# Optimization experiments

Measured on AMD Instinct MI355X. Metric: run time of the kernel, lower is better.

## Reference

```python
import jax, jax.numpy as jnp
import numpy as np

B = 131072      # flattened batch of item embeddings
E = 256         # e_dim; x has 2*E features (src half, rec half)
NQ = 4          # residual quantizer levels per branch
NE = 256        # codebook size per level
BETA = 0.25


def setup_inputs() -> dict:
    key = jax.random.key(0)
    k1, k2, k3 = jax.random.split(key, 3)
    x = jax.random.normal(k1, (B, 2 * E), dtype=jnp.float32)
    src_codebooks = jax.random.normal(k2, (NQ, NE, E), dtype=jnp.float32)
    rec_codebooks = jax.random.normal(k3, (NQ, NE, E), dtype=jnp.float32)
    return {"x": x, "src_codebooks": src_codebooks, "rec_codebooks": rec_codebooks}


def _vq(residual, cb):
    # residual: [B, E], cb: [NE, E]
    # squared euclidean distances via expanded form (GEMM-dominated)
    d = (jnp.sum(residual * residual, axis=1, keepdims=True)
         - 2.0 * (residual @ cb.T)
         + jnp.sum(cb * cb, axis=1)[None, :])          # [B, NE]
    idx = jnp.argmin(d, axis=1)                          # [B]
    x_q = cb[idx]                                        # gather [B, E]
    loss = (jnp.mean((jax.lax.stop_gradient(x_q) - residual) ** 2)
            + BETA * jnp.mean((x_q - jax.lax.stop_gradient(residual)) ** 2))
    # straight-through estimator
    x_q = residual + jax.lax.stop_gradient(x_q - residual)
    return x_q, loss, idx


def _rq(x_part, codebooks):
    # sequential residual VQ chain over NQ levels (small fixed unroll)
    residual = x_part
    x_q = jnp.zeros_like(x_part)
    losses, indices = [], []
    for i in range(codebooks.shape[0]):
        x_res, l, idx = _vq(residual, codebooks[i])
        residual = residual - x_res
        x_q = x_q + x_res
        losses.append(l)
        indices.append(idx)
    return x_q, jnp.stack(losses), jnp.stack(indices, axis=-1)


def reference(x, src_codebooks, rec_codebooks):
    src_x_q, src_l, src_idx = _rq(x[:, :E], src_codebooks)
    rec_x_q, rec_l, rec_idx = _rq(x[:, E:], rec_codebooks)
    mean_loss = jnp.mean(jnp.concatenate([src_l, rec_l]))
    return ((src_x_q, rec_x_q), mean_loss, (src_idx, rec_idx))
```

## Files before the change

### kernel.cpp

```cpp
#include <hip/hip_runtime.h>
#include <hip/hip_bf16.h>
#include <hip/hip_fp16.h>
#include <cstdint>
#include <cstddef>

#define NB   131072
#define ED   256
#define NQL  4
#define NEC  256

typedef _Float16 f16;
typedef f16  f16x8 __attribute__((ext_vector_type(8)));
typedef float f32x4 __attribute__((ext_vector_type(4)));

static constexpr float FMAXV = 3.402823466e+38f;
static constexpr float TAU   = 0.15625f;

static constexpr size_t OFF_REC  = (size_t)NB * ED;
static constexpr size_t OFF_LOSS = 2 * (size_t)NB * ED;
static constexpr size_t OFF_SIDX = OFF_LOSS + 1;
static constexpr size_t OFF_RIDX = OFF_SIDX + (size_t)NB * NQL;

static constexpr size_t WS_LOSS = 0;
static constexpr size_t WS_NORM = 256;
static constexpr size_t WS_CBH  = 256 + 8 * 256 * 4;

__global__ void kPrep(const float* __restrict__ cbS, const float* __restrict__ cbR,
                      float* __restrict__ norms, double* __restrict__ lossAcc) {
  const int cbi = blockIdx.x;
  const int j   = threadIdx.x;
  if (cbi == 0 && j < 8) lossAcc[j] = 0.0;
  const float* row = (cbi < 4 ? cbS : cbR) + ((size_t)(cbi & 3) * NEC + j) * ED;
  float acc = 0.f;
  for (int k = 0; k < ED; k += 4) {
    float4 v = *(const float4*)(row + k);
    acc += v.x * v.x + v.y * v.y + v.z * v.z + v.w * v.w;
  }
  norms[cbi * NEC + j] = acc - 256.0f;
}

__global__ void kConvH(const float* __restrict__ cbS, const float* __restrict__ cbR,
                       f16* __restrict__ cbH) {
  const int f   = blockIdx.x * 256 + threadIdx.x;
  const int cbi = f >> 16;
  const int rem = f & 65535;
  const float v = (cbi < 4 ? cbS + ((size_t)cbi << 16) : cbR + ((size_t)(cbi - 4) << 16))[rem];
  cbH[f] = (f16)v;
}

__device__ __forceinline__ float pk(float v, int j) {
  return __uint_as_float((__float_as_uint(v) & ~255u) | (unsigned)j);
}
__device__ __forceinline__ float unpv(float k) {
  return __uint_as_float(__float_as_uint(k) & ~255u);
}
__device__ __forceinline__ void ins3(float& s0, float& s1, float& s2, float k) {
  float t0 = fmaxf(s0, k); s0 = fminf(s0, k);
  float t1 = fmaxf(s1, t0); s1 = fminf(s1, t0);
  s2 = fminf(s2, t1);
}
__device__ __forceinline__ void mrg3(float& a0, float& a1, float& a2,
                                     float b0, float b1, float b2) {
  float x  = fmaxf(a0, b0);
  float c0 = fminf(a0, b0);
  float m1 = fminf(a1, b1), M1 = fmaxf(a1, b1);
  float c1 = fminf(fminf(x, a1), b1);
  float c2 = fminf(fminf(fmaxf(x, m1), M1), fminf(a2, b2));
  a0 = c0; a1 = c1; a2 = c2;
}

__global__ __launch_bounds__(256, 2)
void kMain(const float* __restrict__ x,
           const float* __restrict__ cbS,
           const float* __restrict__ cbR,
           const f16*  __restrict__ cbH,
           const float* __restrict__ norms,
           double* __restrict__ lossAcc,
           float* __restrict__ out) {
  __shared__ __align__(16) char  RhBuf[64 * 512];
  __shared__ __align__(16) float keybuf[64][4][4];
  __shared__ float redS[4];

  const int tid   = threadIdx.x;
  const int lane  = tid & 63;
  const int w     = tid >> 6;
  const int it_o  = tid >> 2;
  const int kq    = tid & 3;
  const int b0    = blockIdx.x * 64;
  const int l15   = lane & 15;
  const int l4    = lane >> 4;

  float res[64];
  float lossReg = 0.f;

#pragma unroll 1
  for (int br = 0; br < 2; ++br) {
    const float* cbf32 = br ? cbR : cbS;

    {
      const float* xp = x + (size_t)(b0 + it_o) * (2 * ED) + br * ED + kq * 64;
#pragma unroll
      for (int i = 0; i < 16; ++i) {
        float4 v = *(const float4*)(xp + 4 * i);
        res[4 * i + 0] = v.x; res[4 * i + 1] = v.y;
        res[4 * i + 2] = v.z; res[4 * i + 3] = v.w;
      }
    }

#pragma unroll 1
    for (int lev = 0; lev < NQL; ++lev) {
      const int cbi = br * 4 + lev;
      const float* nrm = norms + (size_t)cbi * NEC;

#pragma unroll
      for (int c = 0; c < 8; ++c) {
        f16x8 h;
#pragma unroll
        for (int u = 0; u < 8; ++u) h[u] = (f16)res[c * 8 + u];
        int off = it_o * 512 + kq * 128 + c * 16;
        off ^= (it_o & 7) << 4;
        *(f16x8*)&RhBuf[off] = h;
      }
      __syncthreads();

      const f16* cbh = cbH + ((size_t)cbi << 16);

      f32x4 acc[4][4];
#pragma unroll
      for (int mt = 0; mt < 4; ++mt)
#pragma unroll
        for (int nt = 0; nt < 4; ++nt) { f32x4 z = {0.f, 0.f, 0.f, 0.f}; acc[mt][nt] = z; }

#pragma unroll 2
      for (int ks = 0; ks < 8; ++ks) {
        f16x8 A[4], Bf[4];
#pragma unroll
        for (int mt = 0; mt < 4; ++mt) {
          const int it = mt * 16 + l15;
          const int offA = (it * 512 + ks * 64 + l4 * 16) ^ ((it & 7) << 4);
          A[mt] = *(const f16x8*)&RhBuf[offA];
        }
#pragma unroll
        for (int nt = 0; nt < 4; ++nt) {
          const int j = (w * 4 + nt) * 16 + l15;
          Bf[nt] = *(const f16x8*)&cbh[(size_t)j * ED + ks * 32 + l4 * 8];
        }
#pragma unroll
        for (int mt = 0; mt < 4; ++mt)
#pragma unroll
          for (int nt = 0; nt < 4; ++nt)
            acc[mt][nt] = __builtin_amdgcn_mfma_f32_16x16x32_f16(Bf[nt], A[mt], acc[mt][nt], 0, 0, 0);
      }

      float4 nvq[4];
#pragma unroll
      for (int nt = 0; nt < 4; ++nt)
        nvq[nt] = *(const float4*)&nrm[(w * 4 + nt) * 16 + l4 * 4];

#pragma unroll
      for (int mt = 0; mt < 4; ++mt) {
        float s0 = FMAXV, s1 = FMAXV, s2 = FMAXV;
#pragma unroll
        for (int nt = 0; nt < 4; ++nt) {
#pragma unroll
          for (int r = 0; r < 4; ++r) {
            const int j = (w * 4 + nt) * 16 + l4 * 4 + r;
            const float nr = (r == 0 ? nvq[nt].x : r == 1 ? nvq[nt].y
                              : r == 2 ? nvq[nt].z : nvq[nt].w);
            ins3(s0, s1, s2, pk(fmaf(-2.f, acc[mt][nt][r], nr), j));
          }
        }
        {
          float b0k = __shfl_xor(s0, 16), b1k = __shfl_xor(s1, 16), b2k = __shfl_xor(s2, 16);
          mrg3(s0, s1, s2, b0k, b1k, b2k);
          b0k = __shfl_xor(s0, 32); b1k = __shfl_xor(s1, 32); b2k = __shfl_xor(s2, 32);
          mrg3(s0, s1, s2, b0k, b1k, b2k);
        }
        if (l4 == 0) {
          float4 v; v.x = s0; v.y = s1; v.z = s2; v.w = FMAXV;
          *(float4*)&keybuf[mt * 16 + l15][w][0] = v;
        }
      }
      __syncthreads();

      int jm;
      {
        float4 v = *(const float4*)&keybuf[it_o][kq][0];
        float s0 = v.x, s1 = v.y, s2 = v.z;
        {
          float b0k = __shfl_xor(s0, 1), b1k = __shfl_xor(s1, 1), b2k = __shfl_xor(s2, 1);
          mrg3(s0, s1, s2, b0k, b1k, b2k);
          b0k = __shfl_xor(s0, 2); b1k = __shfl_xor(s1, 2); b2k = __shfl_xor(s2, 2);
          mrg3(s0, s1, s2, b0k, b1k, b2k);
        }
        jm = (int)(__float_as_uint(s0) & 255u);
        const float gap = unpv(s1) - unpv(s0);
        if (gap < TAU) {
          const int cand[3] = { jm,
                                (int)(__float_as_uint(s1) & 255u),
                                (int)(__float_as_uint(s2) & 255u) };
          float bestd = FMAXV; int bestj = 0;
#pragma unroll 1
          for (int cc = 0; cc < 3; ++cc) {
            const int j = cand[cc];
            const float* row = cbf32 + ((size_t)lev * NEC + j) * ED + kq * 64;
            float p = 0.f;
#pragma unroll
            for (int i = 0; i < 16; ++i) {
              float4 q = *(const float4*)(row + 4 * i);
              p = fmaf(res[4 * i + 0], q.x, p);
              p = fmaf(res[4 * i + 1], q.y, p);
              p = fmaf(res[4 * i + 2], q.z, p);
              p = fmaf(res[4 * i + 3], q.w, p);
            }
            p += __shfl_xor(p, 1);
            p += __shfl_xor(p, 2);
            const float d = fmaf(-2.f, p, nrm[j]);
            if (d < bestd || (d == bestd && j < bestj)) { bestd = d; bestj = j; }
          }
          jm = bestj;
        }
        if (kq == 0) {
          const size_t ioff = (br ? OFF_RIDX : OFF_SIDX) + (size_t)(b0 + it_o) * NQL + lev;
          out[ioff] = (float)jm;
        }
      }

      {
        const float* crow = cbf32 + ((size_t)lev * NEC + jm) * ED + kq * 64;
#pragma unroll
        for (int i = 0; i < 16; ++i) {
          float4 q = *(const float4*)(crow + 4 * i);
#pragma unroll
          for (int u = 0; u < 4; ++u) {
            float cv = (u == 0 ? q.x : u == 1 ? q.y : u == 2 ? q.z : q.w);
            float r  = res[4 * i + u];
            float dd = cv - r;
            lossReg = fmaf(dd, dd, lossReg);
            float xr = r + dd;
            res[4 * i + u] = r - xr;
          }
        }
      }
    }

    {
      const float* xp = x + (size_t)(b0 + it_o) * (2 * ED) + br * ED + kq * 64;
      float* op = out + (br ? OFF_REC : 0) + (size_t)(b0 + it_o) * ED + kq * 64;
#pragma unroll
      for (int i = 0; i < 16; ++i) {
        float4 xv = *(const float4*)(xp + 4 * i);
        float4 o;
        o.x = xv.x - res[4 * i + 0];
        o.y = xv.y - res[4 * i + 1];
        o.z = xv.z - res[4 * i + 2];
        o.w = xv.w - res[4 * i + 3];
        *(float4*)(op + 4 * i) = o;
      }
    }
  }

#pragma unroll
  for (int d = 1; d < 64; d <<= 1) lossReg += __shfl_xor(lossReg, d);
  if (lane == 0) redS[w] = lossReg;
  __syncthreads();
  if (tid == 0)
    atomicAdd(&lossAcc[0], (double)((redS[0] + redS[1]) + (redS[2] + redS[3])));
}

__global__ void kFin(const double* __restrict__ lossAcc, float* __restrict__ out) {
  if (blockIdx.x == 0 && threadIdx.x == 0) {
    out[OFF_LOSS] = (float)(lossAcc[0] * 1.25 / ((double)NB * ED) / 8.0);
  }
}

extern "C" void kernel_launch(void* const* d_in, const int* in_sizes, int n_in,
                              void* d_out, int out_size, void* d_ws, size_t ws_size,
                              hipStream_t stream) {
  const float* x   = (const float*)d_in[0];
  const float* cbS = (const float*)d_in[1];
  const float* cbR = (const float*)d_in[2];
  float* out = (float*)d_out;
  char*  ws  = (char*)d_ws;

  double* lossAcc = (double*)(ws + WS_LOSS);
  float*  norms   = (float*)(ws + WS_NORM);
  f16*    cbH     = (f16*)(ws + WS_CBH);

  hipLaunchKernelGGL(kPrep,  dim3(8),    dim3(256), 0, stream, cbS, cbR, norms, lossAcc);
  hipLaunchKernelGGL(kConvH, dim3(2048), dim3(256), 0, stream, cbS, cbR, cbH);
  hipLaunchKernelGGL(kMain,  dim3(NB / 64), dim3(256), 0, stream,
                     x, cbS, cbR, cbH, norms, lossAcc, out);
  hipLaunchKernelGGL(kFin,   dim3(1),    dim3(64),  0, stream, lossAcc, out);
}
```

Before: 580.8 us.

## Halve rows per block to cut registers and raise occupancy to three blocks

Each block now handles 32 rows instead of 64, with 8 threads per row owning 32 features each. This halves the per-thread residual register array and the MFMA accumulator tile, and shrinks LDS buffers. Launch bounds now request 3 blocks per CU, and the grid doubles, with the aim of more waves in flight to hide latency. In exchange, each codebook fragment loaded from global/L2 is reused over half as many rows, which doubles codebook traffic per row. The k-loop unroll drops to 1 and an extra barrier is added between branches.

```diff
diff --git a/kernel.cpp b/kernel.cpp
--- a/kernel.cpp
+++ b/kernel.cpp
@@ -69,7 +69,7 @@
   a0 = c0; a1 = c1; a2 = c2;
 }
 
-__global__ __launch_bounds__(256, 2)
+__global__ __launch_bounds__(256, 3)
 void kMain(const float* __restrict__ x,
            const float* __restrict__ cbS,
            const float* __restrict__ cbR,
@@ -77,20 +77,20 @@
            const float* __restrict__ norms,
            double* __restrict__ lossAcc,
            float* __restrict__ out) {
-  __shared__ __align__(16) char  RhBuf[64 * 512];
-  __shared__ __align__(16) float keybuf[64][4][4];
+  __shared__ __align__(16) char  RhBuf[32 * 512];
+  __shared__ __align__(16) float keybuf[32][4][4];
   __shared__ float redS[4];
 
   const int tid   = threadIdx.x;
   const int lane  = tid & 63;
   const int w     = tid >> 6;
-  const int it_o  = tid >> 2;
-  const int kq    = tid & 3;
-  const int b0    = blockIdx.x * 64;
+  const int it_o  = tid >> 3;
+  const int kg    = tid & 7;
+  const int b0    = blockIdx.x * 32;
   const int l15   = lane & 15;
   const int l4    = lane >> 4;
 
-  float res[64];
+  float res[32];
   float lossReg = 0.f;
 
 #pragma unroll 1
@@ -98,9 +98,9 @@
     const float* cbf32 = br ? cbR : cbS;
 
     {
-      const float* xp = x + (size_t)(b0 + it_o) * (2 * ED) + br * ED + kq * 64;
-#pragma unroll
-      for (int i = 0; i < 16; ++i) {
+      const float* xp = x + (size_t)(b0 + it_o) * (2 * ED) + br * ED + kg * 32;
+#pragma unroll
+      for (int i = 0; i < 8; ++i) {
         float4 v = *(const float4*)(xp + 4 * i);
         res[4 * i + 0] = v.x; res[4 * i + 1] = v.y;
         res[4 * i + 2] = v.z; res[4 * i + 3] = v.w;
@@ -111,62 +111,56 @@
     for (int lev = 0; lev < NQL; ++lev) {
       const int cbi = br * 4 + lev;
       const float* nrm = norms + (size_t)cbi * NEC;
-
-#pragma unroll
-      for (int c = 0; c < 8; ++c) {
+      const f16*   cbh = cbH + ((size_t)cbi << 16);
+
+#pragma unroll
+      for (int c = 0; c < 4; ++c) {
         f16x8 h;
 #pragma unroll
         for (int u = 0; u < 8; ++u) h[u] = (f16)res[c * 8 + u];
-        int off = it_o * 512 + kq * 128 + c * 16;
+        int off = it_o * 512 + kg * 64 + c * 16;
         off ^= (it_o & 7) << 4;
         *(f16x8*)&RhBuf[off] = h;
       }
       __syncthreads();
 
-      const f16* cbh = cbH + ((size_t)cbi << 16);
-
-      f32x4 acc[4][4];
-#pragma unroll
-      for (int mt = 0; mt < 4; ++mt)
+      f32x4 acc[2][4];
+#pragma unroll
+      for (int mt = 0; mt < 2; ++mt)
 #pragma unroll
         for (int nt = 0; nt < 4; ++nt) { f32x4 z = {0.f, 0.f, 0.f, 0.f}; acc[mt][nt] = z; }
 
-#pragma unroll 2
+#pragma unroll 1
       for (int ks = 0; ks < 8; ++ks) {
-        f16x8 A[4], Bf[4];
-#pragma unroll
-        for (int mt = 0; mt < 4; ++mt) {
+        f16x8 A[2], Bf[4];
+#pragma unroll
+        for (int mt = 0; mt < 2; ++mt) {
           const int it = mt * 16 + l15;
           const int offA = (it * 512 + ks * 64 + l4 * 16) ^ ((it & 7) << 4);
           A[mt] = *(const f16x8*)&RhBuf[offA];
         }
 #pragma unroll
         for (int nt = 0; nt < 4; ++nt) {
-          const int j = (w * 4 + nt) * 16 + l15;
+          const int j = w * 64 + nt * 16 + l15;
           Bf[nt] = *(const f16x8*)&cbh[(size_t)j * ED + ks * 32 + l4 * 8];
         }
 #pragma unroll
-        for (int mt = 0; mt < 4; ++mt)
+        for (int mt = 0; mt < 2; ++mt)
 #pragma unroll
           for (int nt = 0; nt < 4; ++nt)
             acc[mt][nt] = __builtin_amdgcn_mfma_f32_16x16x32_f16(Bf[nt], A[mt], acc[mt][nt], 0, 0, 0);
       }
 
-      float4 nvq[4];
-#pragma unroll
-      for (int nt = 0; nt < 4; ++nt)
-        nvq[nt] = *(const float4*)&nrm[(w * 4 + nt) * 16 + l4 * 4];
-
-#pragma unroll
-      for (int mt = 0; mt < 4; ++mt) {
+#pragma unroll
+      for (int mt = 0; mt < 2; ++mt) {
         float s0 = FMAXV, s1 = FMAXV, s2 = FMAXV;
 #pragma unroll
         for (int nt = 0; nt < 4; ++nt) {
+          const float4 nv4 = *(const float4*)&nrm[w * 64 + nt * 16 + l4 * 4];
 #pragma unroll
           for (int r = 0; r < 4; ++r) {
-            const int j = (w * 4 + nt) * 16 + l4 * 4 + r;
-            const float nr = (r == 0 ? nvq[nt].x : r == 1 ? nvq[nt].y
-                              : r == 2 ? nvq[nt].z : nvq[nt].w);
+            const int j = w * 64 + nt * 16 + l4 * 4 + r;
+            const float nr = (r == 0 ? nv4.x : r == 1 ? nv4.y : r == 2 ? nv4.z : nv4.w);
             ins3(s0, s1, s2, pk(fmaf(-2.f, acc[mt][nt][r], nr), j));
           }
         }
@@ -185,7 +179,8 @@
 
       int jm;
       {
-        float4 v = *(const float4*)&keybuf[it_o][kq][0];
+        const int kq4 = kg & 3;
+        float4 v = *(const float4*)&keybuf[it_o][kq4][0];
         float s0 = v.x, s1 = v.y, s2 = v.z;
         {
           float b0k = __shfl_xor(s0, 1), b1k = __shfl_xor(s1, 1), b2k = __shfl_xor(s2, 1);
@@ -203,33 +198,34 @@
 #pragma unroll 1
           for (int cc = 0; cc < 3; ++cc) {
             const int j = cand[cc];
-            const float* row = cbf32 + ((size_t)lev * NEC + j) * ED + kq * 64;
-            float p = 0.f;
-#pragma unroll
-            for (int i = 0; i < 16; ++i) {
+            const float* row = cbf32 + ((size_t)lev * NEC + j) * ED + kg * 32;
+            float p2 = 0.f;
+#pragma unroll
+            for (int i = 0; i < 8; ++i) {
               float4 q = *(const float4*)(row + 4 * i);
-              p = fmaf(res[4 * i + 0], q.x, p);
-              p = fmaf(res[4 * i + 1], q.y, p);
-              p = fmaf(res[4 * i + 2], q.z, p);
-              p = fmaf(res[4 * i + 3], q.w, p);
+              p2 = fmaf(res[4 * i + 0], q.x, p2);
+              p2 = fmaf(res[4 * i + 1], q.y, p2);
+              p2 = fmaf(res[4 * i + 2], q.z, p2);
+              p2 = fmaf(res[4 * i + 3], q.w, p2);
             }
-            p += __shfl_xor(p, 1);
-            p += __shfl_xor(p, 2);
-            const float d = fmaf(-2.f, p, nrm[j]);
+            p2 += __shfl_xor(p2, 1);
+            p2 += __shfl_xor(p2, 2);
+            p2 += __shfl_xor(p2, 4);
+            const float d = fmaf(-2.f, p2, nrm[j]);
             if (d < bestd || (d == bestd && j < bestj)) { bestd = d; bestj = j; }
           }
           jm = bestj;
         }
-        if (kq == 0) {
+        if (kg == 0) {
           const size_t ioff = (br ? OFF_RIDX : OFF_SIDX) + (size_t)(b0 + it_o) * NQL + lev;
           out[ioff] = (float)jm;
         }
       }
 
       {
-        const float* crow = cbf32 + ((size_t)lev * NEC + jm) * ED + kq * 64;
-#pragma unroll
-        for (int i = 0; i < 16; ++i) {
+        const float* crow = cbf32 + ((size_t)lev * NEC + jm) * ED + kg * 32;
+#pragma unroll
+        for (int i = 0; i < 8; ++i) {
           float4 q = *(const float4*)(crow + 4 * i);
 #pragma unroll
           for (int u = 0; u < 4; ++u) {
@@ -245,10 +241,10 @@
     }
 
     {
-      const float* xp = x + (size_t)(b0 + it_o) * (2 * ED) + br * ED + kq * 64;
-      float* op = out + (br ? OFF_REC : 0) + (size_t)(b0 + it_o) * ED + kq * 64;
-#pragma unroll
-      for (int i = 0; i < 16; ++i) {
+      const float* xp = x + (size_t)(b0 + it_o) * (2 * ED) + br * ED + kg * 32;
+      float* op = out + (br ? OFF_REC : 0) + (size_t)(b0 + it_o) * ED + kg * 32;
+#pragma unroll
+      for (int i = 0; i < 8; ++i) {
         float4 xv = *(const float4*)(xp + 4 * i);
         float4 o;
         o.x = xv.x - res[4 * i + 0];
@@ -258,6 +254,7 @@
         *(float4*)(op + 4 * i) = o;
       }
     }
+    __syncthreads();
   }
 
 #pragma unroll
@@ -289,7 +286,7 @@
 
   hipLaunchKernelGGL(kPrep,  dim3(8),    dim3(256), 0, stream, cbS, cbR, norms, lossAcc);
   hipLaunchKernelGGL(kConvH, dim3(2048), dim3(256), 0, stream, cbS, cbR, cbH);
-  hipLaunchKernelGGL(kMain,  dim3(NB / 64), dim3(256), 0, stream,
+  hipLaunchKernelGGL(kMain,  dim3(NB / 32), dim3(256), 0, stream,
                      x, cbS, cbR, cbH, norms, lossAcc, out);
   hipLaunchKernelGGL(kFin,   dim3(1),    dim3(64),  0, stream, lossAcc, out);
 }
```

Result: slower. 735.6 us (+26.7%).
